# Kernel optimization log

Hardware: AMD Instinct MI355X
Metric: run time of the kernel (lower is better)

Reference implementation:

```python
import jax, jax.numpy as jnp
import numpy as np
from jax import lax

B, CIN, H, W = 32, 256, 28, 28
COUT, KS, KEXP = 256, 3, 4
HIDDEN = int(CIN * 0.25)  # ratio hard-coded to 0.25 in the module


def setup_inputs() -> dict:
    key = jax.random.key(0)
    k1, k2, k3, k4 = jax.random.split(key, 4)
    x = jax.random.normal(k1, (B, CIN, H, W), dtype=jnp.float32)
    # SE (InvertedEx) params: fc1 (1x1 conv, no bias), fc2 (1x1 conv, bias)
    fc1_w = jax.random.normal(k2, (HIDDEN, CIN), dtype=jnp.float32) * np.float32(np.sqrt(2.0 / CIN))
    fc2_w = jax.random.normal(k3, (KEXP * COUT, HIDDEN), dtype=jnp.float32) * np.float32(np.sqrt(2.0 / HIDDEN))
    fc2_b = jnp.zeros((KEXP * COUT,), dtype=jnp.float32)
    # K expert conv kernels, he_std = sqrt(2) * (CIN*KS^2)^-0.5
    he_std = np.float32(np.sqrt(2.0) * (CIN * KS * KS) ** -0.5)
    weight = jax.random.normal(k4, (KEXP, COUT, CIN, KS, KS), dtype=jnp.float32) * he_std
    return {"x": x, "fc1_w": fc1_w, "fc2_w": fc2_w, "fc2_b": fc2_b, "weight": weight}


def reference(x, fc1_w, fc2_w, fc2_b, weight):
    # --- SE routing ---
    pooled = jnp.mean(x, axis=(2, 3))                        # [B, CIN]
    h = jax.nn.relu(pooled @ fc1_w.T)                        # [B, HIDDEN]
    y = (h @ fc2_w.T + fc2_b).reshape(B, KEXP, COUT)         # [B, K, COUT]
    prob = jax.nn.softmax(y / jnp.sqrt(jnp.float32(HIDDEN)), axis=1)  # softmax over K
    # --- aggregate per-sample kernels ---
    agg_w = jnp.einsum('bko,koihw->boihw', prob, weight)     # [B, COUT, CIN, KS, KS]
    # --- per-sample conv (batched implicit GEMM via vmap) ---
    def conv1(xi, wi):
        return lax.conv_general_dilated(
            xi[None], wi, window_strides=(1, 1), padding=((1, 1), (1, 1)),
            dimension_numbers=('NCHW', 'OIHW', 'NCHW'))[0]
    out = jax.vmap(conv1)(x, agg_w)                          # [B, COUT, H, W]
    return out
```

## Files before the change

kernel.cpp:

```cpp
#include <hip/hip_runtime.h>
#include <math.h>

#define B_    32
#define CIN_  256
#define HW_   784
#define H_    28
#define W_    28
#define COUT_ 256
#define KEXP_ 4
#define HID_  64

typedef short short8 __attribute__((ext_vector_type(8)));
typedef float floatx16 __attribute__((ext_vector_type(16)));

__device__ __forceinline__ unsigned short f2bf(float f) {
    union { float f; unsigned int u; } v; v.f = f;
    unsigned int r = (v.u + 0x7FFFu + ((v.u >> 16) & 1u)) >> 16;
    return (unsigned short)r;
}

__global__ __launch_bounds__(256) void pool_kernel(const float* __restrict__ x,
                                                   float* __restrict__ pooled) {
    int w = blockIdx.x * 4 + (threadIdx.x >> 6);
    int lane = threadIdx.x & 63;
    const float* p = x + (size_t)w * HW_;
    float s = 0.f;
    for (int i = lane; i < HW_; i += 64) s += p[i];
    for (int off = 32; off; off >>= 1) s += __shfl_down(s, off);
    if (lane == 0) pooled[w] = s * (1.0f / HW_);
}

__global__ __launch_bounds__(256) void se_kernel(const float* __restrict__ pooled,
                                                 const float* __restrict__ fc1_w,
                                                 const float* __restrict__ fc2_w,
                                                 const float* __restrict__ fc2_b,
                                                 float* __restrict__ prob) {
    __shared__ float pl[CIN_];
    __shared__ float h[HID_];
    int b = blockIdx.x, t = threadIdx.x;
    pl[t] = pooled[b * CIN_ + t];
    __syncthreads();
    if (t < HID_) {
        float s = 0.f;
        const float* wr = fc1_w + t * CIN_;
        for (int c = 0; c < CIN_; ++c) s += pl[c] * wr[c];
        h[t] = fmaxf(s, 0.f);
    }
    __syncthreads();
    int o = t;
    float yk[KEXP_];
    for (int k = 0; k < KEXP_; ++k) {
        int r = k * COUT_ + o;
        float s = fc2_b[r];
        const float* wr = fc2_w + r * HID_;
        for (int j = 0; j < HID_; ++j) s += h[j] * wr[j];
        yk[k] = s * 0.125f;
    }
    float m = yk[0];
    for (int k = 1; k < KEXP_; ++k) m = fmaxf(m, yk[k]);
    float e[KEXP_], sum = 0.f;
    for (int k = 0; k < KEXP_; ++k) { e[k] = expf(yk[k] - m); sum += e[k]; }
    float inv = 1.0f / sum;
    for (int k = 0; k < KEXP_; ++k)
        prob[b * (KEXP_ * COUT_) + k * COUT_ + o] = e[k] * inv;
}

__global__ __launch_bounds__(256) void xpose_kernel(const float* __restrict__ x,
                                                    unsigned short* __restrict__ x_t) {
    __shared__ float tile[32][33];
    int bid = blockIdx.x;
    int b   = bid / 200;
    int rem = bid - b * 200;
    int ic0 = (rem / 25) * 32;
    int px0 = (rem % 25) * 32;
    int t = threadIdx.x;
    int c = t & 31, rr = t >> 5;
    #pragma unroll
    for (int r = 0; r < 4; ++r) {
        int icr = rr + r * 8;
        int px = px0 + c;
        float v = (px < HW_) ? x[((size_t)(b * CIN_ + ic0 + icr)) * HW_ + px] : 0.f;
        tile[icr][c] = v;
    }
    __syncthreads();
    #pragma unroll
    for (int r = 0; r < 4; ++r) {
        int pxr = rr + r * 8;
        int px = px0 + pxr;
        if (px < HW_)
            x_t[((size_t)b * HW_ + px) * CIN_ + ic0 + c] = f2bf(tile[c][pxr]);
    }
}

__global__ __launch_bounds__(256) void agg_kernel(const float* __restrict__ weight,
                                                  const float* __restrict__ prob,
                                                  unsigned short* __restrict__ agg) {
    __shared__ float ws_w[KEXP_ * CIN_ * 9];
    __shared__ float pb[KEXP_][B_];
    int oc = blockIdx.x, t = threadIdx.x;
    for (int e = t; e < KEXP_ * CIN_ * 9; e += 256) {
        int k = e / (CIN_ * 9);
        int r = e - k * (CIN_ * 9);
        ws_w[e] = weight[((size_t)(k * COUT_ + oc)) * (CIN_ * 9) + r];
    }
    if (t < KEXP_ * B_) {
        int k = t >> 5, b = t & 31;
        pb[k][b] = prob[b * (KEXP_ * COUT_) + k * COUT_ + oc];
    }
    __syncthreads();
    int ic = t;
    for (int rs = 0; rs < 9; ++rs) {
        float w0 = ws_w[0 * CIN_ * 9 + ic * 9 + rs];
        float w1 = ws_w[1 * CIN_ * 9 + ic * 9 + rs];
        float w2 = ws_w[2 * CIN_ * 9 + ic * 9 + rs];
        float w3 = ws_w[3 * CIN_ * 9 + ic * 9 + rs];
        for (int b = 0; b < B_; ++b) {
            float s = pb[0][b] * w0 + pb[1][b] * w1 + pb[2][b] * w2 + pb[3][b] * w3;
            agg[(((size_t)b * 9 + rs) * COUT_ + oc) * CIN_ + ic] = f2bf(s);
        }
    }
}

__global__ __launch_bounds__(256, 3) void conv_mfma_kernel(const unsigned short* __restrict__ x_t,
                                                           const unsigned short* __restrict__ agg,
                                                           float* __restrict__ out) {
    __shared__ __align__(16) short Xs[6 * 35 * 72];
    __shared__ __align__(16) short As[128 * 72];

    int gid = blockIdx.x;
    int rowblk = gid >> 6;
    int pair = gid & 63;
    int b = pair >> 1;
    int oc0 = (pair & 1) * 128;
    int py0 = rowblk * 4;

    int t = threadIdx.x;
    int lane = t & 63, w = t >> 6;
    int ml = lane & 31, kh = lane >> 5;

    floatx16 acc[4];
    #pragma unroll
    for (int j = 0; j < 4; ++j)
        #pragma unroll
        for (int r = 0; r < 16; ++r) acc[j][r] = 0.f;

    const unsigned short* xtb = x_t + (size_t)b * HW_ * CIN_;

    for (int ic0 = 0; ic0 < CIN_; ic0 += 64) {
        __syncthreads();
        #pragma unroll
        for (int i = 0; i < 7; ++i) {
            int l = t + i * 256;
            if (l < 6 * 35 * 8) {
                int pos = l >> 3, g = l & 7;
                int row = pos / 35, col = pos - row * 35;
                int gy = py0 - 1 + row, gx = col - 1;
                short8 v = (short8)0;
                if ((unsigned)gy < 28u && (unsigned)gx < 28u)
                    v = *(const short8*)(xtb + ((size_t)(gy * W_ + gx)) * CIN_ + ic0 + g * 8);
                *(short8*)&Xs[pos * 72 + g * 8] = v;
            }
        }
        for (int rs = 0; rs < 9; ++rs) {
            int dy = rs / 3, dx = rs - dy * 3;
            if (rs) __syncthreads();
            const unsigned short* ag = agg + ((((size_t)b * 9 + rs) * COUT_ + oc0)) * CIN_ + ic0;
            #pragma unroll
            for (int i = 0; i < 4; ++i) {
                int l = t + i * 256;
                int row = l >> 3, g = l & 7;
                *(short8*)&As[row * 72 + g * 8] = *(const short8*)(ag + (size_t)row * CIN_ + g * 8);
            }
            __syncthreads();
            #pragma unroll
            for (int kk = 0; kk < 4; ++kk) {
                short8 a = *(const short8*)&As[(w * 32 + ml) * 72 + kk * 16 + kh * 8];
                #pragma unroll
                for (int j = 0; j < 4; ++j) {
                    short8 bf = *(const short8*)&Xs[((j + dy) * 35 + (ml + dx)) * 72 + kk * 16 + kh * 8];
                    acc[j] = __builtin_amdgcn_mfma_f32_32x32x16_bf16(a, bf, acc[j], 0, 0, 0);
                }
            }
        }
    }

    int col = ml;
    if (col < W_) {
        #pragma unroll
        for (int j = 0; j < 4; ++j) {
            int y = py0 + j;
            #pragma unroll
            for (int r = 0; r < 16; ++r) {
                int ocg = oc0 + w * 32 + (r & 3) + 8 * (r >> 2) + 4 * kh;
                out[((size_t)(b * COUT_ + ocg)) * HW_ + y * W_ + col] = acc[j][r];
            }
        }
    }
}

__global__ __launch_bounds__(256) void conv_kernel(const float* __restrict__ x,
                                                   const float* __restrict__ weight,
                                                   const float* __restrict__ prob,
                                                   float* __restrict__ out) {
    __shared__ float xs[30 * 30];
    __shared__ float wagg[8][32][12];
    __shared__ float pl[KEXP_][8];

    int b  = blockIdx.x >> 5;
    int o0 = (blockIdx.x & 31) * 8;
    int t  = threadIdx.x;

    if (t < 32) {
        int k = t >> 3, oc = t & 7;
        pl[k][oc] = prob[b * (KEXP_ * COUT_) + k * COUT_ + o0 + oc];
    }
    int p0 = t;
    int pr[4], pc[4];
    bool pv[4];
    #pragma unroll
    for (int j = 0; j < 4; ++j) {
        int p = p0 + j * 256;
        pv[j] = p < HW_;
        pr[j] = p / W_;
        pc[j] = p % W_;
    }
    float acc[8][4];
    #pragma unroll
    for (int oc = 0; oc < 8; ++oc)
        #pragma unroll
        for (int j = 0; j < 4; ++j) acc[oc][j] = 0.f;

    int aoc = t >> 5, aii = t & 31;

    for (int ic0 = 0; ic0 < CIN_; ic0 += 32) {
        __syncthreads();
        {
            float w9[9];
            #pragma unroll
            for (int j = 0; j < 9; ++j) w9[j] = 0.f;
            int i = ic0 + aii;
            #pragma unroll
            for (int k = 0; k < KEXP_; ++k) {
                float pk = pl[k][aoc];
                const float* wp = weight + ((size_t)(k * COUT_ + o0 + aoc) * CIN_ + i) * 9;
                #pragma unroll
                for (int j = 0; j < 9; ++j) w9[j] += pk * wp[j];
            }
            #pragma unroll
            for (int j = 0; j < 9; ++j) wagg[aoc][aii][j] = w9[j];
        }
        for (int ii = 0; ii < 32; ++ii) {
            int i = ic0 + ii;
            __syncthreads();
            const float* xp = x + (size_t)(b * CIN_ + i) * HW_;
            for (int e = t; e < 900; e += 256) {
                int ry = e / 30, cx = e - ry * 30;
                int gy = ry - 1, gx = cx - 1;
                float v = 0.f;
                if ((unsigned)gy < 28u && (unsigned)gx < 28u) v = xp[gy * W_ + gx];
                xs[e] = v;
            }
            __syncthreads();
            float xv[4][9];
            #pragma unroll
            for (int j = 0; j < 4; ++j) {
                if (pv[j]) {
                    const float* xr = &xs[pr[j] * 30 + pc[j]];
                    xv[j][0] = xr[0];  xv[j][1] = xr[1];  xv[j][2] = xr[2];
                    xv[j][3] = xr[30]; xv[j][4] = xr[31]; xv[j][5] = xr[32];
                    xv[j][6] = xr[60]; xv[j][7] = xr[61]; xv[j][8] = xr[62];
                } else {
                    #pragma unroll
                    for (int q = 0; q < 9; ++q) xv[j][q] = 0.f;
                }
            }
            #pragma unroll
            for (int oc = 0; oc < 8; ++oc) {
                float4 wa = *(const float4*)&wagg[oc][ii][0];
                float4 wb = *(const float4*)&wagg[oc][ii][4];
                float  wc = wagg[oc][ii][8];
                #pragma unroll
                for (int j = 0; j < 4; ++j) {
                    acc[oc][j] += xv[j][0] * wa.x + xv[j][1] * wa.y + xv[j][2] * wa.z
                                + xv[j][3] * wa.w + xv[j][4] * wb.x + xv[j][5] * wb.y
                                + xv[j][6] * wb.z + xv[j][7] * wb.w + xv[j][8] * wc;
                }
            }
        }
    }
    #pragma unroll
    for (int oc = 0; oc < 8; ++oc) {
        float* op = out + (size_t)(b * COUT_ + o0 + oc) * HW_ + p0;
        #pragma unroll
        for (int j = 0; j < 4; ++j)
            if (pv[j]) op[j * 256] = acc[oc][j];
    }
}

extern "C" void kernel_launch(void* const* d_in, const int* in_sizes, int n_in,
                              void* d_out, int out_size, void* d_ws, size_t ws_size,
                              hipStream_t stream) {
    const float* x     = (const float*)d_in[0];
    const float* fc1_w = (const float*)d_in[1];
    const float* fc2_w = (const float*)d_in[2];
    const float* fc2_b = (const float*)d_in[3];
    const float* weight= (const float*)d_in[4];
    float* out = (float*)d_out;

    char* ws = (char*)d_ws;
    float* pooled = (float*)(ws);
    float* prob   = (float*)(ws + 32768);
    unsigned short* x_t = (unsigned short*)(ws + 163840);
    unsigned short* agg = (unsigned short*)(ws + 13008896);
    const size_t WS_NEED = 50757632;

    pool_kernel<<<(B_ * CIN_) / 4, 256, 0, stream>>>(x, pooled);
    se_kernel<<<B_, 256, 0, stream>>>(pooled, fc1_w, fc2_w, fc2_b, prob);

    if (ws_size >= WS_NEED) {
        xpose_kernel<<<B_ * 8 * 25, 256, 0, stream>>>(x, x_t);
        agg_kernel<<<COUT_, 256, 0, stream>>>(weight, prob, agg);
        conv_mfma_kernel<<<7 * 64, 256, 0, stream>>>(x_t, agg, out);
    } else {
        conv_kernel<<<B_ * (COUT_ / 8), 256, 0, stream>>>(x, weight, prob, out);
    }
}
```

Before: 169.5 us.

## Fuse pooling into transpose, stage SE weights in LDS, split agg, double-buffer conv

Global average pooling moves into the transpose kernel, where each tile's partial sums are added into pooled with atomics after a memset. This removes one full read of x and one launch. The SE kernel now stages fc1/fc2 weights into padded shared memory so the dot-product reads are coalesced. The aggregation kernel is split over 4x more blocks (8 batches each) to raise parallelism. The conv kernel double-buffers the per-tap weight tile, prefetching the next tap into registers during the MFMAs, which cuts barriers but lowers occupancy to 2 blocks/CU and makes the pooled sums order-dependent through float atomics.

```diff
diff --git a/kernel.cpp b/kernel.cpp
--- a/kernel.cpp
+++ b/kernel.cpp
@@ -17,6 +17,40 @@
     union { float f; unsigned int u; } v; v.f = f;
     unsigned int r = (v.u + 0x7FFFu + ((v.u >> 16) & 1u)) >> 16;
     return (unsigned short)r;
+}
+
+__global__ __launch_bounds__(256) void xpose_pool_kernel(const float* __restrict__ x,
+                                                         unsigned short* __restrict__ x_t,
+                                                         float* __restrict__ pooled) {
+    __shared__ float tile[32][33];
+    int bid = blockIdx.x;
+    int b   = bid / 200;
+    int rem = bid - b * 200;
+    int ic0 = (rem / 25) * 32;
+    int px0 = (rem % 25) * 32;
+    int t = threadIdx.x;
+    int c = t & 31, rr = t >> 5;
+    #pragma unroll
+    for (int r = 0; r < 4; ++r) {
+        int icr = rr + r * 8;
+        int px = px0 + c;
+        float v = (px < HW_) ? x[((size_t)(b * CIN_ + ic0 + icr)) * HW_ + px] : 0.f;
+        tile[icr][c] = v;
+    }
+    __syncthreads();
+    #pragma unroll
+    for (int r = 0; r < 4; ++r) {
+        int pxr = rr + r * 8;
+        int px = px0 + pxr;
+        if (px < HW_)
+            x_t[((size_t)b * HW_ + px) * CIN_ + ic0 + c] = f2bf(tile[c][pxr]);
+    }
+    if (t < 32) {
+        float s = 0.f;
+        #pragma unroll
+        for (int cc = 0; cc < 32; ++cc) s += tile[t][cc];
+        atomicAdd(&pooled[b * CIN_ + ic0 + t], s * (1.0f / HW_));
+    }
 }
 
 __global__ __launch_bounds__(256) void pool_kernel(const float* __restrict__ x,
@@ -30,29 +64,46 @@
     if (lane == 0) pooled[w] = s * (1.0f / HW_);
 }
 
-__global__ __launch_bounds__(256) void se_kernel(const float* __restrict__ pooled,
-                                                 const float* __restrict__ fc1_w,
-                                                 const float* __restrict__ fc2_w,
-                                                 const float* __restrict__ fc2_b,
-                                                 float* __restrict__ prob) {
+__global__ __launch_bounds__(256) void se2_kernel(const float* __restrict__ pooled,
+                                                  const float* __restrict__ fc1_w,
+                                                  const float* __restrict__ fc2_w,
+                                                  const float* __restrict__ fc2_b,
+                                                  float* __restrict__ prob) {
     __shared__ float pl[CIN_];
     __shared__ float h[HID_];
+    __shared__ float wb[16640];
     int b = blockIdx.x, t = threadIdx.x;
     pl[t] = pooled[b * CIN_ + t];
+    #pragma unroll
+    for (int i = 0; i < 16; ++i) {
+        int l = t + i * 256;
+        float4 v = *(const float4*)(fc1_w + (size_t)l * 4);
+        int r = l >> 6, cc = (l & 63) * 4;
+        float* dst = &wb[r * 257 + cc];
+        dst[0] = v.x; dst[1] = v.y; dst[2] = v.z; dst[3] = v.w;
+    }
     __syncthreads();
     if (t < HID_) {
         float s = 0.f;
-        const float* wr = fc1_w + t * CIN_;
+        const float* wr = &wb[t * 257];
         for (int c = 0; c < CIN_; ++c) s += pl[c] * wr[c];
         h[t] = fmaxf(s, 0.f);
     }
-    __syncthreads();
-    int o = t;
     float yk[KEXP_];
     for (int k = 0; k < KEXP_; ++k) {
-        int r = k * COUT_ + o;
-        float s = fc2_b[r];
-        const float* wr = fc2_w + r * HID_;
+        __syncthreads();
+        #pragma unroll
+        for (int i = 0; i < 16; ++i) {
+            int l = t + i * 256;
+            float4 v = *(const float4*)(fc2_w + (size_t)k * COUT_ * HID_ + (size_t)l * 4);
+            int o = l >> 4, jj = (l & 15) * 4;
+            float* dst = &wb[o * 65 + jj];
+            dst[0] = v.x; dst[1] = v.y; dst[2] = v.z; dst[3] = v.w;
+        }
+        __syncthreads();
+        float s = fc2_b[k * COUT_ + t];
+        const float* wr = &wb[t * 65];
+        #pragma unroll
         for (int j = 0; j < HID_; ++j) s += h[j] * wr[j];
         yk[k] = s * 0.125f;
     }
@@ -62,50 +113,26 @@
     for (int k = 0; k < KEXP_; ++k) { e[k] = expf(yk[k] - m); sum += e[k]; }
     float inv = 1.0f / sum;
     for (int k = 0; k < KEXP_; ++k)
-        prob[b * (KEXP_ * COUT_) + k * COUT_ + o] = e[k] * inv;
-}
-
-__global__ __launch_bounds__(256) void xpose_kernel(const float* __restrict__ x,
-                                                    unsigned short* __restrict__ x_t) {
-    __shared__ float tile[32][33];
+        prob[b * (KEXP_ * COUT_) + k * COUT_ + t] = e[k] * inv;
+}
+
+__global__ __launch_bounds__(256) void agg2_kernel(const float* __restrict__ weight,
+                                                   const float* __restrict__ prob,
+                                                   unsigned short* __restrict__ agg) {
+    __shared__ float ws_w[KEXP_ * CIN_ * 9];
+    __shared__ float pb[KEXP_][8];
     int bid = blockIdx.x;
-    int b   = bid / 200;
-    int rem = bid - b * 200;
-    int ic0 = (rem / 25) * 32;
-    int px0 = (rem % 25) * 32;
+    int oc = bid & 255;
+    int b0 = (bid >> 8) * 8;
     int t = threadIdx.x;
-    int c = t & 31, rr = t >> 5;
-    #pragma unroll
-    for (int r = 0; r < 4; ++r) {
-        int icr = rr + r * 8;
-        int px = px0 + c;
-        float v = (px < HW_) ? x[((size_t)(b * CIN_ + ic0 + icr)) * HW_ + px] : 0.f;
-        tile[icr][c] = v;
-    }
-    __syncthreads();
-    #pragma unroll
-    for (int r = 0; r < 4; ++r) {
-        int pxr = rr + r * 8;
-        int px = px0 + pxr;
-        if (px < HW_)
-            x_t[((size_t)b * HW_ + px) * CIN_ + ic0 + c] = f2bf(tile[c][pxr]);
-    }
-}
-
-__global__ __launch_bounds__(256) void agg_kernel(const float* __restrict__ weight,
-                                                  const float* __restrict__ prob,
-                                                  unsigned short* __restrict__ agg) {
-    __shared__ float ws_w[KEXP_ * CIN_ * 9];
-    __shared__ float pb[KEXP_][B_];
-    int oc = blockIdx.x, t = threadIdx.x;
     for (int e = t; e < KEXP_ * CIN_ * 9; e += 256) {
         int k = e / (CIN_ * 9);
         int r = e - k * (CIN_ * 9);
         ws_w[e] = weight[((size_t)(k * COUT_ + oc)) * (CIN_ * 9) + r];
     }
-    if (t < KEXP_ * B_) {
-        int k = t >> 5, b = t & 31;
-        pb[k][b] = prob[b * (KEXP_ * COUT_) + k * COUT_ + oc];
+    if (t < KEXP_ * 8) {
+        int k = t >> 3, bb = t & 7;
+        pb[k][bb] = prob[(b0 + bb) * (KEXP_ * COUT_) + k * COUT_ + oc];
     }
     __syncthreads();
     int ic = t;
@@ -114,18 +141,19 @@
         float w1 = ws_w[1 * CIN_ * 9 + ic * 9 + rs];
         float w2 = ws_w[2 * CIN_ * 9 + ic * 9 + rs];
         float w3 = ws_w[3 * CIN_ * 9 + ic * 9 + rs];
-        for (int b = 0; b < B_; ++b) {
-            float s = pb[0][b] * w0 + pb[1][b] * w1 + pb[2][b] * w2 + pb[3][b] * w3;
-            agg[(((size_t)b * 9 + rs) * COUT_ + oc) * CIN_ + ic] = f2bf(s);
-        }
-    }
-}
-
-__global__ __launch_bounds__(256, 3) void conv_mfma_kernel(const unsigned short* __restrict__ x_t,
-                                                           const unsigned short* __restrict__ agg,
-                                                           float* __restrict__ out) {
+        #pragma unroll
+        for (int bb = 0; bb < 8; ++bb) {
+            float s = pb[0][bb] * w0 + pb[1][bb] * w1 + pb[2][bb] * w2 + pb[3][bb] * w3;
+            agg[(((size_t)(b0 + bb) * 9 + rs) * COUT_ + oc) * CIN_ + ic] = f2bf(s);
+        }
+    }
+}
+
+__global__ __launch_bounds__(256, 2) void conv_mfma2_kernel(const unsigned short* __restrict__ x_t,
+                                                            const unsigned short* __restrict__ agg,
+                                                            float* __restrict__ out) {
     __shared__ __align__(16) short Xs[6 * 35 * 72];
-    __shared__ __align__(16) short As[128 * 72];
+    __shared__ __align__(16) short As[2][128 * 72];
 
     int gid = blockIdx.x;
     int rowblk = gid >> 6;
@@ -145,9 +173,11 @@
         for (int r = 0; r < 16; ++r) acc[j][r] = 0.f;
 
     const unsigned short* xtb = x_t + (size_t)b * HW_ * CIN_;
+    const unsigned short* agb = agg + ((size_t)b * 9 * COUT_ + oc0) * CIN_;
+
+    int arow = t >> 3, ag = t & 7;
 
     for (int ic0 = 0; ic0 < CIN_; ic0 += 64) {
-        __syncthreads();
         #pragma unroll
         for (int i = 0; i < 7; ++i) {
             int l = t + i * 256;
@@ -161,26 +191,44 @@
                 *(short8*)&Xs[pos * 72 + g * 8] = v;
             }
         }
+        {
+            const unsigned short* ap = agb + ic0 + (size_t)ag * 8;
+            #pragma unroll
+            for (int i = 0; i < 4; ++i) {
+                short8 v = *(const short8*)(ap + (size_t)(arow + i * 32) * CIN_);
+                *(short8*)&As[0][(arow + i * 32) * 72 + ag * 8] = v;
+            }
+        }
+        __syncthreads();
+
         for (int rs = 0; rs < 9; ++rs) {
+            int cur = rs & 1;
             int dy = rs / 3, dx = rs - dy * 3;
-            if (rs) __syncthreads();
-            const unsigned short* ag = agg + ((((size_t)b * 9 + rs) * COUT_ + oc0)) * CIN_ + ic0;
-            #pragma unroll
-            for (int i = 0; i < 4; ++i) {
-                int l = t + i * 256;
-                int row = l >> 3, g = l & 7;
-                *(short8*)&As[row * 72 + g * 8] = *(const short8*)(ag + (size_t)row * CIN_ + g * 8);
-            }
-            __syncthreads();
+            short8 rv0, rv1, rv2, rv3;
+            if (rs < 8) {
+                const unsigned short* ap = agb + (size_t)(rs + 1) * COUT_ * CIN_ + ic0 + (size_t)ag * 8;
+                rv0 = *(const short8*)(ap + (size_t)(arow +  0) * CIN_);
+                rv1 = *(const short8*)(ap + (size_t)(arow + 32) * CIN_);
+                rv2 = *(const short8*)(ap + (size_t)(arow + 64) * CIN_);
+                rv3 = *(const short8*)(ap + (size_t)(arow + 96) * CIN_);
+            }
             #pragma unroll
             for (int kk = 0; kk < 4; ++kk) {
-                short8 a = *(const short8*)&As[(w * 32 + ml) * 72 + kk * 16 + kh * 8];
+                short8 a = *(const short8*)&As[cur][(w * 32 + ml) * 72 + kk * 16 + kh * 8];
                 #pragma unroll
                 for (int j = 0; j < 4; ++j) {
                     short8 bf = *(const short8*)&Xs[((j + dy) * 35 + (ml + dx)) * 72 + kk * 16 + kh * 8];
                     acc[j] = __builtin_amdgcn_mfma_f32_32x32x16_bf16(a, bf, acc[j], 0, 0, 0);
                 }
             }
+            if (rs < 8) {
+                short* dst = &As[cur ^ 1][arow * 72 + ag * 8];
+                *(short8*)(dst +  0 * 72)      = rv0;
+                *(short8*)(dst + 32 * 72)      = rv1;
+                *(short8*)(dst + 64 * 72)      = rv2;
+                *(short8*)(dst + 96 * 72)      = rv3;
+            }
+            __syncthreads();
         }
     }
 
@@ -277,13 +325,13 @@
             #pragma unroll
             for (int oc = 0; oc < 8; ++oc) {
                 float4 wa = *(const float4*)&wagg[oc][ii][0];
-                float4 wb = *(const float4*)&wagg[oc][ii][4];
+                float4 wb2 = *(const float4*)&wagg[oc][ii][4];
                 float  wc = wagg[oc][ii][8];
                 #pragma unroll
                 for (int j = 0; j < 4; ++j) {
                     acc[oc][j] += xv[j][0] * wa.x + xv[j][1] * wa.y + xv[j][2] * wa.z
-                                + xv[j][3] * wa.w + xv[j][4] * wb.x + xv[j][5] * wb.y
-                                + xv[j][6] * wb.z + xv[j][7] * wb.w + xv[j][8] * wc;
+                                + xv[j][3] * wa.w + xv[j][4] * wb2.x + xv[j][5] * wb2.y
+                                + xv[j][6] * wb2.z + xv[j][7] * wb2.w + xv[j][8] * wc;
                 }
             }
         }
@@ -314,14 +362,15 @@
     unsigned short* agg = (unsigned short*)(ws + 13008896);
     const size_t WS_NEED = 50757632;
 
-    pool_kernel<<<(B_ * CIN_) / 4, 256, 0, stream>>>(x, pooled);
-    se_kernel<<<B_, 256, 0, stream>>>(pooled, fc1_w, fc2_w, fc2_b, prob);
-
     if (ws_size >= WS_NEED) {
-        xpose_kernel<<<B_ * 8 * 25, 256, 0, stream>>>(x, x_t);
-        agg_kernel<<<COUT_, 256, 0, stream>>>(weight, prob, agg);
-        conv_mfma_kernel<<<7 * 64, 256, 0, stream>>>(x_t, agg, out);
+        hipMemsetAsync(pooled, 0, B_ * CIN_ * sizeof(float), stream);
+        xpose_pool_kernel<<<B_ * 8 * 25, 256, 0, stream>>>(x, x_t, pooled);
+        se2_kernel<<<B_, 256, 0, stream>>>(pooled, fc1_w, fc2_w, fc2_b, prob);
+        agg2_kernel<<<4 * COUT_, 256, 0, stream>>>(weight, prob, agg);
+        conv_mfma2_kernel<<<7 * 64, 256, 0, stream>>>(x_t, agg, out);
     } else {
+        pool_kernel<<<(B_ * CIN_) / 4, 256, 0, stream>>>(x, pooled);
+        se2_kernel<<<B_, 256, 0, stream>>>(pooled, fc1_w, fc2_w, fc2_b, prob);
         conv_kernel<<<B_ * (COUT_ / 8), 256, 0, stream>>>(x, weight, prob, out);
     }
 }
```

Result: faster. 156.8 us (-7.5%).
